# Optimization experiments

Measured on AMD Instinct MI355X. Metric: run time of the kernel, lower is better.

Reference implementation:

```python
import jax, jax.numpy as jnp
import numpy as np

B, T, H, OUT_LEN, D_IN, D_OUT = 512, 512, 256, 8, 64, 64

def _lstm_seq(x, Wih, Whh, bih, bhh):
    # batch_first LSTM, zero initial state; x: [B,T,D] -> [B,T,H]
    b = bih + bhh
    h0 = jnp.zeros((x.shape[0], Whh.shape[1]), x.dtype)
    def step(carry, xt):
        h, c = carry
        g = xt @ Wih.T + h @ Whh.T + b
        i, f, gg, o = jnp.split(g, 4, axis=-1)  # torch gate order i,f,g,o
        c = jax.nn.sigmoid(f) * c + jax.nn.sigmoid(i) * jnp.tanh(gg)
        h = jax.nn.sigmoid(o) * jnp.tanh(c)
        return (h, c), h
    _, hs = jax.lax.scan(step, (h0, h0), jnp.swapaxes(x, 0, 1))
    return jnp.swapaxes(hs, 0, 1)

def _lstm_cell0(xt, Wih, bih, bhh):
    # single decode step; original calls self.dec with fresh zero (h,c) each
    # step, so the recurrent matrix Whh never contributes.
    g = xt @ Wih.T + bih + bhh
    i, f, gg, o = jnp.split(g, 4, axis=-1)
    c = jax.nn.sigmoid(i) * jnp.tanh(gg)
    return jax.nn.sigmoid(o) * jnp.tanh(c)

def _mlp(x, Ws, bs, Wl, bl):
    # simple.mlp: hidden Linear+ReLU stack, linear output (dropout off)
    for k in range(Ws.shape[0]):
        x = jax.nn.relu(x @ Ws[k] + bs[k])
    return x @ Wl + bl

def setup_inputs():
    key = jax.random.key(0)
    ks = iter(jax.random.split(key, 32))
    def W(shape, fan):
        return jax.random.normal(next(ks), shape, jnp.float32) / np.float32(np.sqrt(fan))
    return {
        'x': jax.random.normal(next(ks), (B, T, D_IN), jnp.float32),
        'in_W': W((D_IN, H), D_IN), 'in_b': jnp.zeros((H,), jnp.float32),
        'enc_Wih': W((4*H, H), H), 'enc_Whh': W((4*H, H), H),
        'enc_bih': jnp.zeros((4*H,), jnp.float32), 'enc_bhh': jnp.zeros((4*H,), jnp.float32),
        'dec_Wih': W((4*H, 2*H), 2*H), 'dec_Whh': W((4*H, H), H),
        'dec_bih': jnp.zeros((4*H,), jnp.float32), 'dec_bhh': jnp.zeros((4*H,), jnp.float32),
        'w_Ws': W((3, H, H), H), 'w_bs': jnp.zeros((3, H), jnp.float32), 'w_Wl': W((H, H), H), 'w_bl': jnp.zeros((H,), jnp.float32),
        'u_Ws': W((3, H, H), H), 'u_bs': jnp.zeros((3, H), jnp.float32), 'u_Wl': W((H, H), H), 'u_bl': jnp.zeros((H,), jnp.float32),
        'v_Ws': W((7, H, H), H), 'v_bs': jnp.zeros((7, H), jnp.float32), 'v_Wl': W((H, 1), H), 'v_bl': jnp.zeros((1,), jnp.float32),
        'out_W': W((H, D_OUT), H), 'out_b': jnp.zeros((D_OUT,), jnp.float32),
    }

def reference(x, in_W, in_b, enc_Wih, enc_Whh, enc_bih, enc_bhh,
              dec_Wih, dec_Whh, dec_bih, dec_bhh,
              w_Ws, w_bs, w_Wl, w_bl, u_Ws, u_bs, u_Wl, u_bl,
              v_Ws, v_bs, v_Wl, v_bl, out_W, out_b):
    h = x @ in_W + in_b                                       # input projection [B,T,H]
    enc = _lstm_seq(h, enc_Wih, enc_Whh, enc_bih, enc_bhh)    # [B,T,H]
    whs = _mlp(enc, w_Ws, w_bs, w_Wl, w_bl)                   # w(hs), loop-invariant (hoisted)
    def dec_step(s, _):
        us = _mlp(s, u_Ws, u_bs, u_Wl, u_bl)                  # [B,H]
        e = _mlp(jnp.tanh(us[:, None, :] + whs), v_Ws, v_bs, v_Wl, v_bl)  # [B,T,1]
        a = jax.nn.softmax(e, axis=1)                         # softmax over time
        c_t = jnp.sum(a * enc, axis=1)                        # [B,H] weighted sum
        s_new = _lstm_cell0(jnp.concatenate([c_t, s], axis=-1), dec_Wih, dec_bih, dec_bhh)
        return s_new, s_new
    s0 = jnp.zeros((x.shape[0], H), x.dtype)
    _, ss = jax.lax.scan(dec_step, s0, None, length=OUT_LEN)  # [OUT_LEN,B,H]
    dec = jnp.swapaxes(ss, 0, 1)                              # [B,OUT_LEN,H]
    return dec @ out_W + out_b                                # output projection
```

## Files before the change

### kernel.cpp

```cpp
#include <hip/hip_runtime.h>
#include <math.h>

#define B_    512
#define T_    512
#define H_    256
#define DIN_  64
#define OL_   8
#define DOUT_ 64

#define CBv   128
#define HSTR  32768

typedef unsigned short u16;
typedef unsigned int u32;
typedef unsigned long long ull;
typedef __attribute__((ext_vector_type(8))) short short8;
typedef __attribute__((ext_vector_type(4))) float f32x4;

static __device__ __forceinline__ float sigm(float x){ return 1.0f/(1.0f + expf(-x)); }
static __device__ __forceinline__ float bf2f(u16 h){
  u32 u = ((u32)h) << 16; float f; __builtin_memcpy(&f, &u, 4); return f;
}
static __device__ __forceinline__ u16 f2bf(float f){
  u32 u; __builtin_memcpy(&u, &f, 4);
  u = (u + 0x7fffu + ((u >> 16) & 1u)) >> 16;
  return (u16)u;
}
static __device__ __forceinline__ u32 packhl(float f){
  u16 h = f2bf(f);
  u16 lo = f2bf(f - bf2f(h));
  return ((u32)h << 16) | (u32)lo;
}
static __device__ __forceinline__ float unpackhl(u32 w){
  return bf2f((u16)(w >> 16)) + bf2f((u16)(w & 0xffff));
}
static __device__ __forceinline__ u32 al(const u32* p){
  return __hip_atomic_load(p, __ATOMIC_RELAXED, __HIP_MEMORY_SCOPE_AGENT);
}
static __device__ __forceinline__ void as_(u32* p, u32 v){
  __hip_atomic_store(p, v, __ATOMIC_RELAXED, __HIP_MEMORY_SCOPE_AGENT);
}

__global__ void k_wpt(const float* __restrict__ inW, const float* __restrict__ Wih,
                      float* __restrict__ WpT)
{
  int gid = blockIdx.x * 256 + threadIdx.x;
  int c = gid >> 6, d = gid & 63;
  const float* wr = Wih + c * H_;
  const float* ir = inW + d * H_;
  float acc = 0.f;
  #pragma unroll 4
  for (int e = 0; e < H_; e += 4) {
    float4 av = *(const float4*)(ir + e);
    float4 bv = *(const float4*)(wr + e);
    acc += av.x*bv.x + av.y*bv.y + av.z*bv.z + av.w*bv.w;
  }
  WpT[c*64 + d] = acc;
}

__global__ void k_bp(const float* __restrict__ inb, const float* __restrict__ Wih,
                     const float* __restrict__ bih, const float* __restrict__ bhh,
                     float* __restrict__ bp)
{
  int c = blockIdx.x * 256 + threadIdx.x;
  const float* wr = Wih + c * H_;
  float acc = bih[c] + bhh[c];
  for (int e = 0; e < H_; ++e) acc += inb[e] * wr[e];
  bp[c] = acc;
}

__global__ void k_dwt(const float* __restrict__ dWih, float* __restrict__ dWt)
{
  int gid = blockIdx.x * 256 + threadIdx.x;
  int j = gid >> 9, k = gid & 511;
  int row = (j < 256) ? j : (j + 256);
  dWt[k*768 + j] = dWih[row*512 + k];
}

__global__ void k_wall(const float* __restrict__ wWs, const float* __restrict__ wWl,
                       const float* __restrict__ uWs, const float* __restrict__ uWl,
                       const float* __restrict__ vWs, u16* __restrict__ outb)
{
  int lyr = blockIdx.y;
  const float* W = (lyr < 3)  ? wWs + lyr*65536
                 : (lyr == 3) ? wWl
                 : (lyr < 7)  ? uWs + (lyr-4)*65536
                 : (lyr == 7) ? uWl
                 :              vWs + (lyr-8)*65536;
  u16* out = outb + (size_t)lyr*131072;
  int gid = blockIdx.x * 256 + threadIdx.x;
  int k = gid & 255, n = gid >> 8;
  float v = W[k*256 + n];
  int s = k >> 5, j = k & 7;
  int lane = (((k >> 3) & 3) << 4) | (n & 15);
  int fl = ((s*16) + (n >> 4))*512 + lane*8 + j;
  u16 h = f2bf(v);
  out[fl] = h;
  out[65536 + fl] = f2bf(v - bf2f(h));
}

__global__ void k_whhfl(const float* __restrict__ Whh, u16* __restrict__ out)
{
  int gid = blockIdx.x * 256 + threadIdx.x;
  int j = gid & 7, l = (gid >> 3) & 63, ctg = (gid >> 9) & 63, s = gid >> 15;
  int k = s*32 + (l >> 4)*8 + j;
  int wv = ctg >> 2, g = ctg & 3;
  int row = g*256 + wv*16 + (l & 15);
  float v = Whh[row*256 + k];
  int fl = (s*64 + ctg)*512 + l*8 + j;
  u16 h = f2bf(v);
  out[fl] = h;
  out[262144 + fl] = f2bf(v - bf2f(h));
}

__global__ void k_wpfl(const float* __restrict__ WpT, u16* __restrict__ out)
{
  int gid = blockIdx.x * 256 + threadIdx.x;
  int j = gid & 7, l = (gid >> 3) & 63, ctg = (gid >> 9) & 63, s = gid >> 15;
  int k = s*32 + (l >> 4)*8 + j;
  int wv = ctg >> 2, g = ctg & 3;
  int row = g*256 + wv*16 + (l & 15);
  float v = WpT[row*64 + k];
  int fl = (s*64 + ctg)*512 + l*8 + j;
  u16 h = f2bf(v);
  out[fl] = h;
  out[65536 + fl] = f2bf(v - bf2f(h));
}

__global__ __launch_bounds__(256,1) void k_enc(
    const float* __restrict__ x, const u16* __restrict__ whhFL,
    const u16* __restrict__ wpFL, const float* __restrict__ bp,
    u32* __restrict__ henc)
{
  __shared__ float G[2][16][32][4];
  const int tid = threadIdx.x, l = tid & 63, wv = tid >> 6;
  const int lr = l & 15, lk = l >> 4;
  const int rg = blockIdx.x, bg = blockIdx.y, z = blockIdx.z;
  const int ug2 = wv >> 1;
  const int g0 = (wv & 1) * 2;
  const int u16g = bg*2 + ug2;

  short8 whH[8][2], whL[8][2], wpH[2][2], wpL[2][2];
  #pragma unroll
  for (int s = 0; s < 8; ++s)
    #pragma unroll
    for (int c = 0; c < 2; ++c) {
      int ctg = u16g*4 + g0 + c;
      whH[s][c] = *(const short8*)(whhFL + ((size_t)(s*64 + ctg))*512 + l*8);
      whL[s][c] = *(const short8*)(whhFL + 262144 + ((size_t)(s*64 + ctg))*512 + l*8);
    }
  #pragma unroll
  for (int s = 0; s < 2; ++s)
    #pragma unroll
    for (int c = 0; c < 2; ++c) {
      int ctg = u16g*4 + g0 + c;
      wpH[s][c] = *(const short8*)(wpFL + ((size_t)(s*64 + ctg))*512 + l*8);
      wpL[s][c] = *(const short8*)(wpFL + 65536 + ((size_t)(s*64 + ctg))*512 + l*8);
    }
  const int ul = tid & 31, er0 = tid >> 5;
  float bb[4];
  #pragma unroll
  for (int g = 0; g < 4; ++g) bb[g] = bp[g*256 + bg*32 + ul];
  float cs[2] = {0.f, 0.f};

  u32* hz = henc + (size_t)z * (size_t)(T_+1) * HSTR;
  const float* xrow = x + ((size_t)(z*CBv + rg*16 + lr)*T_)*DIN_ + lk*8;

  for (int t = 0; t < T_; ++t) {
    float4 xv0 = *(const float4*)(xrow);
    float4 xv1 = *(const float4*)(xrow + 4);
    float4 xv2 = *(const float4*)(xrow + 32);
    float4 xv3 = *(const float4*)(xrow + 36);
    xrow += DIN_;

    const ull* hb = (const ull*)(hz + (size_t)t*HSTR + (size_t)(rg*16 + lr)*256);
    ull hq[8][4];
    #pragma unroll
    for (int s = 0; s < 8; ++s)
      #pragma unroll
      for (int q = 0; q < 4; ++q)
        hq[s][q] = __hip_atomic_load(hb + s*16 + lk*4 + q,
                                     __ATOMIC_RELAXED, __HIP_MEMORY_SCOPE_AGENT);
    if (t) {
      for (;;) {
        bool ok = true;
        #pragma unroll
        for (int s = 0; s < 8; ++s)
          #pragma unroll
          for (int q = 0; q < 4; ++q) {
            u32 a = (u32)hq[s][q], b = (u32)(hq[s][q] >> 32);
            ok = ok && (a != 0u) && (b != 0u);
          }
        if (__all(ok)) break;
        __builtin_amdgcn_s_sleep(1);
        #pragma unroll
        for (int s = 0; s < 8; ++s)
          #pragma unroll
          for (int q = 0; q < 4; ++q)
            hq[s][q] = __hip_atomic_load(hb + s*16 + lk*4 + q,
                                         __ATOMIC_RELAXED, __HIP_MEMORY_SCOPE_AGENT);
      }
    }

    f32x4 acc[2];
    acc[0] = (f32x4){0.f,0.f,0.f,0.f};
    acc[1] = (f32x4){0.f,0.f,0.f,0.f};

    #pragma unroll
    for (int s = 0; s < 2; ++s) {
      float vv[8];
      if (s == 0) { vv[0]=xv0.x;vv[1]=xv0.y;vv[2]=xv0.z;vv[3]=xv0.w;vv[4]=xv1.x;vv[5]=xv1.y;vv[6]=xv1.z;vv[7]=xv1.w; }
      else        { vv[0]=xv2.x;vv[1]=xv2.y;vv[2]=xv2.z;vv[3]=xv2.w;vv[4]=xv3.x;vv[5]=xv3.y;vv[6]=xv3.z;vv[7]=xv3.w; }
      short8 ah, al2;
      #pragma unroll
      for (int j = 0; j < 8; ++j) {
        u16 h = f2bf(vv[j]);
        ah[j] = (short)h;
        al2[j] = (short)f2bf(vv[j] - bf2f(h));
      }
      #pragma unroll
      for (int c = 0; c < 2; ++c) {
        acc[c] = __builtin_amdgcn_mfma_f32_16x16x32_bf16(ah,  wpH[s][c], acc[c], 0,0,0);
        acc[c] = __builtin_amdgcn_mfma_f32_16x16x32_bf16(al2, wpH[s][c], acc[c], 0,0,0);
        acc[c] = __builtin_amdgcn_mfma_f32_16x16x32_bf16(ah,  wpL[s][c], acc[c], 0,0,0);
      }
    }
    #pragma unroll
    for (int s = 0; s < 8; ++s) {
      short8 ah, al2;
      #pragma unroll
      for (int q = 0; q < 4; ++q) {
        u32 w0 = (u32)hq[s][q], w1 = (u32)(hq[s][q] >> 32);
        ah[q*2]   = (short)(w0 >> 16); al2[q*2]   = (short)(w0 & 0xffff);
        ah[q*2+1] = (short)(w1 >> 16); al2[q*2+1] = (short)(w1 & 0xffff);
      }
      #pragma unroll
      for (int c = 0; c < 2; ++c) {
        acc[c] = __builtin_amdgcn_mfma_f32_16x16x32_bf16(ah,  whH[s][c], acc[c], 0,0,0);
        acc[c] = __builtin_amdgcn_mfma_f32_16x16x32_bf16(al2, whH[s][c], acc[c], 0,0,0);
        acc[c] = __builtin_amdgcn_mfma_f32_16x16x32_bf16(ah,  whL[s][c], acc[c], 0,0,0);
      }
    }

    const int p = t & 1;
    #pragma unroll
    for (int c = 0; c < 2; ++c)
      #pragma unroll
      for (int j = 0; j < 4; ++j)
        G[p][lk*4 + j][ug2*16 + lr][g0 + c] = acc[c][j];
    __syncthreads();

    #pragma unroll
    for (int pp = 0; pp < 2; ++pp) {
      int row = er0 + pp*8;
      float4 gq = *(const float4*)&G[p][row][ul][0];
      float gi = gq.x + bb[0], gf = gq.y + bb[1];
      float gg = gq.z + bb[2], go = gq.w + bb[3];
      float cn = sigm(gf)*cs[pp] + sigm(gi)*tanhf(gg);
      float hn = sigm(go)*tanhf(cn);
      cs[pp] = cn;
      as_(hz + (size_t)(t+1)*HSTR + (size_t)(rg*16 + row)*256 + bg*32 + ul,
          packhl(hn) | 1u);
    }
  }
}

static __device__ __forceinline__ void mlp_core(
    u32* act, const u16* wFL, const float* bs, const float* bl,
    int L, int nbs, bool lastRelu, int tid)
{
  const int l = tid & 63, cg = tid >> 6;
  const int lr = l & 15, lk = l >> 4;
  f32x4 acc[4][2];
  for (int lyr = 0; lyr < L; ++lyr) {
    __syncthreads();
    const u16* wb = wFL + (size_t)lyr*131072;
    #pragma unroll
    for (int rt = 0; rt < 4; ++rt)
      #pragma unroll
      for (int ct = 0; ct < 2; ++ct) acc[rt][ct] = (f32x4){0.f,0.f,0.f,0.f};

    short8 bh[3][2], blo[3][2];
    #pragma unroll
    for (int pre = 0; pre < 2; ++pre)
      #pragma unroll
      for (int ct = 0; ct < 2; ++ct) {
        const u16* bfp = wb + ((size_t)(pre*16 + cg*2 + ct))*512 + l*8;
        bh[pre][ct]  = *(const short8*)bfp;
        blo[pre][ct] = *(const short8*)(bfp + 65536);
      }
    #pragma unroll
    for (int s = 0; s < 8; ++s) {
      const int cur = s % 3, nxt = (s + 2) % 3;
      if (s < 6) {
        #pragma unroll
        for (int ct = 0; ct < 2; ++ct) {
          const u16* bfp = wb + ((size_t)((s+2)*16 + cg*2 + ct))*512 + l*8;
          bh[nxt][ct]  = *(const short8*)bfp;
          blo[nxt][ct] = *(const short8*)(bfp + 65536);
        }
      }
      short8 ah[4], al2[4];
      #pragma unroll
      for (int rt = 0; rt < 4; ++rt) {
        int row = rt*16 + lr;
        int cc = s*8 + lk*2;
        const u32* base = act + row*256;
        uint4 d0 = *(const uint4*)(base + (((cc    ) ^ (row & 7)) << 2));
        uint4 d1 = *(const uint4*)(base + (((cc + 1) ^ (row & 7)) << 2));
        u32 q[8] = {d0.x,d0.y,d0.z,d0.w,d1.x,d1.y,d1.z,d1.w};
        #pragma unroll
        for (int j = 0; j < 8; ++j) {
          ah[rt][j]  = (short)(q[j] >> 16);
          al2[rt][j] = (short)(q[j] & 0xffff);
        }
      }
      #pragma unroll
      for (int ct = 0; ct < 2; ++ct)
        #pragma unroll
        for (int rt = 0; rt < 4; ++rt) {
          acc[rt][ct] = __builtin_amdgcn_mfma_f32_16x16x32_bf16(ah[rt],  bh[cur][ct],  acc[rt][ct], 0,0,0);
          acc[rt][ct] = __builtin_amdgcn_mfma_f32_16x16x32_bf16(al2[rt], bh[cur][ct],  acc[rt][ct], 0,0,0);
          acc[rt][ct] = __builtin_amdgcn_mfma_f32_16x16x32_bf16(ah[rt],  blo[cur][ct], acc[rt][ct], 0,0,0);
        }
    }
    const float* bptr = (lyr < nbs) ? (bs + lyr*256) : bl;
    const bool dorelu = (lyr < L-1) || lastRelu;
    #pragma unroll
    for (int ct = 0; ct < 2; ++ct) {
      float bv = bptr[cg*32 + ct*16 + lr];
      #pragma unroll
      for (int rt = 0; rt < 4; ++rt)
        #pragma unroll
        for (int g = 0; g < 4; ++g) {
          float xv = acc[rt][ct][g] + bv;
          acc[rt][ct][g] = dorelu ? fmaxf(xv, 0.f) : xv;
        }
    }
    __syncthreads();
    #pragma unroll
    for (int ct = 0; ct < 2; ++ct) {
      int n = cg*32 + ct*16 + lr;
      #pragma unroll
      for (int rt = 0; rt < 4; ++rt)
        #pragma unroll
        for (int g = 0; g < 4; ++g) {
          int row = rt*16 + lk*4 + g;
          act[row*256 + (((n >> 2) ^ (row & 7)) << 2) + (n & 3)] = packhl(acc[rt][ct][g]);
        }
    }
  }
  __syncthreads();
}

__global__ __launch_bounds__(512,1) void k_dec_all(
    const u32* __restrict__ henc, const u16* __restrict__ mlpFL,
    const float* __restrict__ wbs, const float* __restrict__ wbl,
    const float* __restrict__ ubs, const float* __restrict__ ubl,
    const float* __restrict__ vbs, const float* __restrict__ vWl,
    const float* __restrict__ vbl,
    const float* __restrict__ dWt, const float* __restrict__ dbih,
    const float* __restrict__ dbhh,
    const float* __restrict__ oW, const float* __restrict__ ob,
    u32* __restrict__ whsP,
    u32* __restrict__ eS, u32* __restrict__ ctxS, u32* __restrict__ sS,
    float* __restrict__ outc)
{
  extern __shared__ u32 act[];
  __shared__ float red[8], red2[8];
  const int bid = blockIdx.x, tid = threadIdx.x;
  u32* usL = act + 16384;
  const u16* wFLw = mlpFL;
  const u16* wFLu = mlpFL + 4*131072;
  const u16* wFLv = mlpFL + 8*131072;
  const int half = bid & 1;
  const bool useW = (whsP != nullptr);
  float sprev[4] = {0.f, 0.f, 0.f, 0.f};

  if (useW) {
    for (int k = 0; k < 4; ++k) {
      long m0t = (long)(bid + 256*k) * 64;
      __syncthreads();
      for (int i = tid; i < 4096; i += 512) {
        int row = i >> 6, c16 = i & 63;
        uint4 pk = *(const uint4*)(henc + HSTR + (m0t + row)*256 + c16*4);
        *((uint4*)(act + row*256 + ((c16 ^ (row & 7)) << 2))) = pk;
      }
      mlp_core(act, wFLw, wbs, wbl, 4, 3, false, tid);
      for (int i = tid; i < 4096; i += 512) {
        int row = i >> 6, c16 = i & 63;
        uint4 pk = *((const uint4*)(act + row*256 + ((c16 ^ (row & 7)) << 2)));
        *(uint4*)(whsP + (m0t + row)*256 + c16*4) = pk;
      }
    }
  }

  for (int s = 0; s < OL_; ++s) {
    __syncthreads();
    for (int i = tid; i < 4096; i += 512) {
      int row = i >> 6, c16 = i & 63;
      uint4 pk;
      if (s) {
        const u32* sp = sS + (size_t)s*32768 + (size_t)(half*64 + row)*256 + c16*4;
        u32 w0 = al(sp), w1 = al(sp+1), w2 = al(sp+2), w3 = al(sp+3);
        while (!(w0 && w1 && w2 && w3)) {
          __builtin_amdgcn_s_sleep(1);
          w0 = al(sp); w1 = al(sp+1); w2 = al(sp+2); w3 = al(sp+3);
        }
        pk = (uint4){ packhl(__uint_as_float(w0)), packhl(__uint_as_float(w1)),
                      packhl(__uint_as_float(w2)), packhl(__uint_as_float(w3)) };
      } else {
        pk = (uint4){0u, 0u, 0u, 0u};
      }
      *((uint4*)(act + row*256 + ((c16 ^ (row & 7)) << 2))) = pk;
    }
    mlp_core(act, wFLu, ubs, ubl, 4, 3, false, tid);
    for (int i = tid; i < 16384; i += 512) usL[i] = act[i];

    for (int k = 0; k < 4; ++k) {
      long m0t = (long)(bid + 256*k) * 64;
      __syncthreads();
      if (useW) {
        for (int i = tid; i < 4096; i += 512) {
          int row = i >> 6, c16 = i & 63;
          uint4 pw = *(const uint4*)(whsP + (m0t + row)*256 + c16*4);
          u32* dst = act + row*256 + ((c16 ^ (row & 7)) << 2);
          const u32* uw = usL + row*256 + ((c16 ^ (row & 7)) << 2);
          dst[0] = packhl(tanhf(unpackhl(pw.x) + unpackhl(uw[0])));
          dst[1] = packhl(tanhf(unpackhl(pw.y) + unpackhl(uw[1])));
          dst[2] = packhl(tanhf(unpackhl(pw.z) + unpackhl(uw[2])));
          dst[3] = packhl(tanhf(unpackhl(pw.w) + unpackhl(uw[3])));
        }
      } else {
        for (int i = tid; i < 4096; i += 512) {
          int row = i >> 6, c16 = i & 63;
          uint4 pk = *(const uint4*)(henc + HSTR + (m0t + row)*256 + c16*4);
          *((uint4*)(act + row*256 + ((c16 ^ (row & 7)) << 2))) = pk;
        }
        mlp_core(act, wFLw, wbs, wbl, 4, 3, false, tid);
        for (int i = tid; i < 16384; i += 512) {
          u32 a = act[i], u = usL[i];
          act[i] = packhl(tanhf(unpackhl(a) + unpackhl(u)));
        }
      }
      mlp_core(act, wFLv, vbs, vbs, 7, 7, true, tid);
      {
        int r2 = tid >> 3, q = tid & 7;
        float p = 0.f;
        #pragma unroll 8
        for (int j = 0; j < 32; ++j) {
          int n = q*32 + j;
          u32 w = act[r2*256 + (((n >> 2) ^ (r2 & 7)) << 2) + (n & 3)];
          p += unpackhl(w) * vWl[n];
        }
        p += __shfl_xor(p, 1, 64);
        p += __shfl_xor(p, 2, 64);
        p += __shfl_xor(p, 4, 64);
        if (q == 0)
          as_(eS + (size_t)s*65536 + m0t + r2, __float_as_uint(p + vbl[0]) | 1u);
      }
    }

    if (bid >= 64 && bid < 192) {
      int b = bid - 64;
      __syncthreads();
      float* asx = (float*)act;
      const u32* ep0 = eS + (size_t)s*65536 + b;
      u32 w0;
      for (;;) {
        w0 = al(ep0 + (size_t)tid*128);
        if (w0) break;
        __builtin_amdgcn_s_sleep(1);
      }
      float v0 = __uint_as_float(w0);
      const int lane = tid & 63, wv = tid >> 6;
      float m = v0;
      #pragma unroll
      for (int o = 32; o; o >>= 1) m = fmaxf(m, __shfl_xor(m, o, 64));
      if (!lane) red[wv] = m;
      __syncthreads();
      m = fmaxf(fmaxf(fmaxf(red[0], red[1]), fmaxf(red[2], red[3])),
                fmaxf(fmaxf(red[4], red[5]), fmaxf(red[6], red[7])));
      float x0 = expf(v0 - m);
      float sm = x0;
      #pragma unroll
      for (int o = 32; o; o >>= 1) sm += __shfl_xor(sm, o, 64);
      if (!lane) red2[wv] = sm;
      __syncthreads();
      float inv = 1.f / (red2[0] + red2[1] + red2[2] + red2[3]
                       + red2[4] + red2[5] + red2[6] + red2[7]);
      asx[tid] = x0 * inv;
      __syncthreads();
      int unit = tid & 255, hf = tid >> 8;
      float accv = 0.f;
      const u32* hp = henc + HSTR + (size_t)b*256 + unit;
      #pragma unroll 8
      for (int t = hf*256; t < hf*256 + 256; ++t)
        accv += asx[t] * unpackhl(hp[(size_t)t*HSTR]);
      float* part = asx + 512;
      part[tid] = accv;
      __syncthreads();
      if (hf == 0)
        as_(ctxS + (size_t)s*32768 + b*256 + unit,
            __float_as_uint(accv + part[256 + unit]) | 1u);
    }

    if (bid >= 224) {
      int c = bid - 224, b0r = c*4;
      __syncthreads();
      float* xt = (float*)act;
      const int u = tid & 255, kh = tid >> 8;
      if (kh == 0) {
        const u32* cp = ctxS + (size_t)s*32768 + (size_t)b0r*256 + u;
        u32 w0, w1, w2, w3;
        for (;;) {
          w0 = al(cp); w1 = al(cp + 256); w2 = al(cp + 512); w3 = al(cp + 768);
          if (w0 && w1 && w2 && w3) break;
          __builtin_amdgcn_s_sleep(1);
        }
        xt[0*520 + u] = __uint_as_float(w0);
        xt[1*520 + u] = __uint_as_float(w1);
        xt[2*520 + u] = __uint_as_float(w2);
        xt[3*520 + u] = __uint_as_float(w3);
        #pragma unroll
        for (int bb = 0; bb < 4; ++bb) xt[bb*520 + 256 + u] = sprev[bb];
      }
      __syncthreads();
      float ai[4], ag[4], ao[4];
      #pragma unroll
      for (int bb = 0; bb < 4; ++bb) { ai[bb]=0.f; ag[bb]=0.f; ao[bb]=0.f; }
      #pragma unroll 4
      for (int k = kh*256; k < kh*256 + 256; ++k) {
        float wi = dWt[k*768 + u];
        float wg = dWt[k*768 + 256 + u];
        float wo = dWt[k*768 + 512 + u];
        #pragma unroll
        for (int bb = 0; bb < 4; ++bb) {
          float xv = xt[bb*520 + k];
          ai[bb] += xv*wi; ag[bb] += xv*wg; ao[bb] += xv*wo;
        }
      }
      float* pr = xt + 4*520;
      if (kh) {
        #pragma unroll
        for (int bb = 0; bb < 4; ++bb) {
          pr[(0*4 + bb)*256 + u] = ai[bb];
          pr[(1*4 + bb)*256 + u] = ag[bb];
          pr[(2*4 + bb)*256 + u] = ao[bb];
        }
      }
      __syncthreads();
      float* sn = pr + 3*4*256;
      if (!kh) {
        float bi = dbih[u]       + dbhh[u];
        float bg = dbih[512 + u] + dbhh[512 + u];
        float bo = dbih[768 + u] + dbhh[768 + u];
        #pragma unroll
        for (int bb = 0; bb < 4; ++bb) {
          float a1 = ai[bb] + pr[(0*4 + bb)*256 + u];
          float g1 = ag[bb] + pr[(1*4 + bb)*256 + u];
          float o1 = ao[bb] + pr[(2*4 + bb)*256 + u];
          float cn = sigm(a1 + bi) * tanhf(g1 + bg);
          float hn = sigm(o1 + bo) * tanhf(cn);
          as_(sS + (size_t)(s+1)*32768 + (size_t)(b0r + bb)*256 + u,
              __float_as_uint(hn) | 1u);
          sprev[bb] = hn;
          sn[bb*256 + u] = hn;
        }
      }
      __syncthreads();
      if (tid < 256) {
        int d = tid & 63, rr = tid >> 6;
        float a2 = ob[d];
        #pragma unroll 4
        for (int k = 0; k < 256; ++k) a2 += sn[rr*256 + k] * oW[k*64 + d];
        outc[((size_t)(b0r + rr)*OL_ + s)*64 + d] = a2;
      }
    }
  }
}

extern "C" void kernel_launch(void* const* d_in, const int* in_sizes, int n_in,
                              void* d_out, int out_size, void* d_ws, size_t ws_size,
                              hipStream_t stream)
{
  (void)in_sizes; (void)n_in;
  const float* x    = (const float*)d_in[0];
  const float* inW  = (const float*)d_in[1];
  const float* inb  = (const float*)d_in[2];
  const float* eWih = (const float*)d_in[3];
  const float* eWhh = (const float*)d_in[4];
  const float* ebih = (const float*)d_in[5];
  const float* ebhh = (const float*)d_in[6];
  const float* dWih = (const float*)d_in[7];
  const float* dbih = (const float*)d_in[9];
  const float* dbhh = (const float*)d_in[10];
  const float* wWs  = (const float*)d_in[11];
  const float* wbs  = (const float*)d_in[12];
  const float* wWl  = (const float*)d_in[13];
  const float* wbl  = (const float*)d_in[14];
  const float* uWs  = (const float*)d_in[15];
  const float* ubs  = (const float*)d_in[16];
  const float* uWl  = (const float*)d_in[17];
  const float* ubl  = (const float*)d_in[18];
  const float* vWs  = (const float*)d_in[19];
  const float* vbs  = (const float*)d_in[20];
  const float* vWl  = (const float*)d_in[21];
  const float* vbl  = (const float*)d_in[22];
  const float* oW   = (const float*)d_in[23];
  const float* ob   = (const float*)d_in[24];
  float* out = (float*)d_out;

  hipFuncSetAttribute((const void*)k_dec_all, hipFuncAttributeMaxDynamicSharedMemorySize, 131072);

  const size_t hsz = (size_t)(T_+1) * HSTR;
  const size_t avail = ws_size / 4;
  const size_t scratchU = 524288ull + 262144 + 294912;
  const size_t prepsU = 1770496ull;
  auto needf = [&](int nc, int usewhs) -> size_t {
    return (size_t)nc*hsz + (usewhs ? 16777216ull : 0ull) + scratchU + prepsU + 4096;
  };
  int NC = 1, USEW = 0;
  if      (needf(4,1) <= avail) { NC = 4; USEW = 1; }
  else if (needf(4,0) <= avail) { NC = 4; USEW = 0; }
  else if (needf(2,1) <= avail) { NC = 2; USEW = 1; }
  else if (needf(1,1) <= avail) { NC = 1; USEW = 1; }
  else if (needf(1,0) <= avail) { NC = 1; USEW = 0; }
  else { hipMemsetAsync(d_out, 0, (size_t)out_size*4, stream); return; }

  float* wsf = (float*)d_ws;
  size_t o = 0;
  u32* henc = (u32*)(wsf + o);  o += (size_t)NC*hsz;
  u32* whsP = nullptr;
  if (USEW) { whsP = (u32*)(wsf + o);  o += 16777216; }
  u32* eS   = (u32*)(wsf + o);  o += 524288;
  u32* ctxS = (u32*)(wsf + o);  o += 262144;
  u32* sS   = (u32*)(wsf + o);  o += 294912;
  float* WpT = wsf + o;  o += 65536;
  float* bp  = wsf + o;  o += 1024;
  float* dWt = wsf + o;  o += 393216;
  u16* whhFL = (u16*)(wsf + o);  o += 262144;
  u16* wpFL  = (u16*)(wsf + o);  o += 65536;
  u16* mlpFL = (u16*)(wsf + o);

  const size_t scratchBytes = scratchU * 4;

  k_wpt<<<256, 256, 0, stream>>>(inW, eWih, WpT);
  k_bp <<<4,   256, 0, stream>>>(inb, eWih, ebih, ebhh, bp);
  k_dwt<<<1536,256, 0, stream>>>(dWih, dWt);
  k_whhfl<<<1024,256,0,stream>>>(eWhh, whhFL);
  k_wpfl <<<256, 256,0,stream>>>(WpT, wpFL);
  k_wall <<<dim3(256,15), 256, 0, stream>>>(wWs, wWl, uWs, uWl, vWs, mlpFL);

  for (int c0 = 0; c0 < B_; c0 += CBv*NC) {
    hipMemsetAsync(henc, 0, (size_t)NC*hsz*4, stream);

    k_enc<<<dim3(CBv/16, 8, NC), 256, 0, stream>>>(
        x + (size_t)c0*T_*DIN_, whhFL, wpFL, bp, henc);

    for (int z = 0; z < NC; ++z) {
      hipMemsetAsync(eS, 0, scratchBytes, stream);
      k_dec_all<<<256, 512, 131072, stream>>>(
          henc + (size_t)z*hsz, mlpFL,
          wbs, wbl, ubs, ubl, vbs, vWl, vbl,
          dWt, dbih, dbhh, oW, ob,
          whsP, eS, ctxS, sS,
          out + (size_t)(c0 + z*CBv)*OL_*DOUT_);
    }
  }
}
```

Measured before the change: 16.64 ms.

## Store MLP activations as split hi/lo bf16 planes in shared memory

Replaces the packed hi|lo u32 activation layout in LDS with two separate bf16 planes, swizzled in 8-element groups. MFMA A operands can then be loaded directly as short8 vectors instead of being unpacked from u32 words on every k-step. All producers and consumers (loads, tanh combine, u-state copy, final dot) are adapted to the new layout. It also stops selecting the 4-chunk encoder configuration and falls back to at most 2 chunks, which may reduce encoder parallelism.

```diff
diff --git a/kernel.cpp b/kernel.cpp
--- a/kernel.cpp
+++ b/kernel.cpp
@@ -266,7 +266,7 @@
 }
 
 static __device__ __forceinline__ void mlp_core(
-    u32* act, const u16* wFL, const float* bs, const float* bl,
+    u16* hi, u16* lo, const u16* wFL, const float* bs, const float* bl,
     int L, int nbs, bool lastRelu, int tid)
 {
   const int l = tid & 63, cg = tid >> 6;
@@ -304,16 +304,9 @@
       #pragma unroll
       for (int rt = 0; rt < 4; ++rt) {
         int row = rt*16 + lr;
-        int cc = s*8 + lk*2;
-        const u32* base = act + row*256;
-        uint4 d0 = *(const uint4*)(base + (((cc    ) ^ (row & 7)) << 2));
-        uint4 d1 = *(const uint4*)(base + (((cc + 1) ^ (row & 7)) << 2));
-        u32 q[8] = {d0.x,d0.y,d0.z,d0.w,d1.x,d1.y,d1.z,d1.w};
-        #pragma unroll
-        for (int j = 0; j < 8; ++j) {
-          ah[rt][j]  = (short)(q[j] >> 16);
-          al2[rt][j] = (short)(q[j] & 0xffff);
-        }
+        int gs = (s*4 + lk) ^ ((row & 7) << 2);
+        ah[rt]  = *(const short8*)(hi + row*256 + gs*8);
+        al2[rt] = *(const short8*)(lo + row*256 + gs*8);
       }
       #pragma unroll
       for (int ct = 0; ct < 2; ++ct)
@@ -346,7 +339,11 @@
         #pragma unroll
         for (int g = 0; g < 4; ++g) {
           int row = rt*16 + lk*4 + g;
-          act[row*256 + (((n >> 2) ^ (row & 7)) << 2) + (n & 3)] = packhl(acc[rt][ct][g]);
+          int a = row*256 + (((n >> 3) ^ ((row & 7) << 2)) << 3) + (n & 7);
+          float xv = acc[rt][ct][g];
+          u16 h = f2bf(xv);
+          hi[a] = h;
+          lo[a] = f2bf(xv - bf2f(h));
         }
     }
   }
@@ -369,7 +366,10 @@
   extern __shared__ u32 act[];
   __shared__ float red[8], red2[8];
   const int bid = blockIdx.x, tid = threadIdx.x;
-  u32* usL = act + 16384;
+  u16* hiA = (u16*)act;
+  u16* loA = hiA + 16384;
+  u16* hiU = hiA + 32768;
+  u16* loU = hiA + 49152;
   const u16* wFLw = mlpFL;
   const u16* wFLu = mlpFL + 4*131072;
   const u16* wFLv = mlpFL + 8*131072;
@@ -381,77 +381,135 @@
     for (int k = 0; k < 4; ++k) {
       long m0t = (long)(bid + 256*k) * 64;
       __syncthreads();
-      for (int i = tid; i < 4096; i += 512) {
-        int row = i >> 6, c16 = i & 63;
-        uint4 pk = *(const uint4*)(henc + HSTR + (m0t + row)*256 + c16*4);
-        *((uint4*)(act + row*256 + ((c16 ^ (row & 7)) << 2))) = pk;
-      }
-      mlp_core(act, wFLw, wbs, wbl, 4, 3, false, tid);
-      for (int i = tid; i < 4096; i += 512) {
-        int row = i >> 6, c16 = i & 63;
-        uint4 pk = *((const uint4*)(act + row*256 + ((c16 ^ (row & 7)) << 2)));
-        *(uint4*)(whsP + (m0t + row)*256 + c16*4) = pk;
+      for (int i = tid; i < 2048; i += 512) {
+        int row = i >> 5, g8 = i & 31;
+        const u32* src = henc + HSTR + (m0t + row)*256 + g8*8;
+        uint4 a0 = *(const uint4*)src, a1 = *(const uint4*)(src + 4);
+        u32 w[8] = {a0.x,a0.y,a0.z,a0.w,a1.x,a1.y,a1.z,a1.w};
+        short8 hv, lv;
+        #pragma unroll
+        for (int j = 0; j < 8; ++j) { hv[j] = (short)(w[j] >> 16); lv[j] = (short)(w[j] & 0xffff); }
+        int gs = g8 ^ ((row & 7) << 2);
+        *(short8*)(hiA + row*256 + gs*8) = hv;
+        *(short8*)(loA + row*256 + gs*8) = lv;
+      }
+      mlp_core(hiA, loA, wFLw, wbs, wbl, 4, 3, false, tid);
+      for (int i = tid; i < 2048; i += 512) {
+        int row = i >> 5, g8 = i & 31;
+        int gs = g8 ^ ((row & 7) << 2);
+        short8 hv = *(const short8*)(hiA + row*256 + gs*8);
+        short8 lv = *(const short8*)(loA + row*256 + gs*8);
+        u32 w[8];
+        #pragma unroll
+        for (int j = 0; j < 8; ++j) w[j] = ((u32)(u16)hv[j] << 16) | (u32)(u16)lv[j];
+        u32* dst = whsP + (m0t + row)*256 + g8*8;
+        *(uint4*)dst       = (uint4){w[0],w[1],w[2],w[3]};
+        *(uint4*)(dst + 4) = (uint4){w[4],w[5],w[6],w[7]};
       }
     }
   }
 
   for (int s = 0; s < OL_; ++s) {
     __syncthreads();
-    for (int i = tid; i < 4096; i += 512) {
-      int row = i >> 6, c16 = i & 63;
-      uint4 pk;
+    for (int i = tid; i < 2048; i += 512) {
+      int row = i >> 5, g8 = i & 31;
+      short8 hv, lv;
       if (s) {
-        const u32* sp = sS + (size_t)s*32768 + (size_t)(half*64 + row)*256 + c16*4;
-        u32 w0 = al(sp), w1 = al(sp+1), w2 = al(sp+2), w3 = al(sp+3);
-        while (!(w0 && w1 && w2 && w3)) {
+        const u32* sp = sS + (size_t)s*32768 + (size_t)(half*64 + row)*256 + g8*8;
+        u32 w[8];
+        for (;;) {
+          bool ok = true;
+          #pragma unroll
+          for (int j = 0; j < 8; ++j) { w[j] = al(sp + j); ok = ok && (w[j] != 0u); }
+          if (ok) break;
           __builtin_amdgcn_s_sleep(1);
-          w0 = al(sp); w1 = al(sp+1); w2 = al(sp+2); w3 = al(sp+3);
-        }
-        pk = (uint4){ packhl(__uint_as_float(w0)), packhl(__uint_as_float(w1)),
-                      packhl(__uint_as_float(w2)), packhl(__uint_as_float(w3)) };
+        }
+        #pragma unroll
+        for (int j = 0; j < 8; ++j) {
+          float v = __uint_as_float(w[j]);
+          u16 h = f2bf(v);
+          hv[j] = (short)h;
+          lv[j] = (short)f2bf(v - bf2f(h));
+        }
       } else {
-        pk = (uint4){0u, 0u, 0u, 0u};
-      }
-      *((uint4*)(act + row*256 + ((c16 ^ (row & 7)) << 2))) = pk;
-    }
-    mlp_core(act, wFLu, ubs, ubl, 4, 3, false, tid);
-    for (int i = tid; i < 16384; i += 512) usL[i] = act[i];
+        #pragma unroll
+        for (int j = 0; j < 8; ++j) { hv[j] = 0; lv[j] = 0; }
+      }
+      int gs = g8 ^ ((row & 7) << 2);
+      *(short8*)(hiA + row*256 + gs*8) = hv;
+      *(short8*)(loA + row*256 + gs*8) = lv;
+    }
+    mlp_core(hiA, loA, wFLu, ubs, ubl, 4, 3, false, tid);
+    for (int i = tid; i < 16384; i += 512) act[16384 + i] = act[i];
+    __syncthreads();
 
     for (int k = 0; k < 4; ++k) {
       long m0t = (long)(bid + 256*k) * 64;
       __syncthreads();
       if (useW) {
-        for (int i = tid; i < 4096; i += 512) {
-          int row = i >> 6, c16 = i & 63;
-          uint4 pw = *(const uint4*)(whsP + (m0t + row)*256 + c16*4);
-          u32* dst = act + row*256 + ((c16 ^ (row & 7)) << 2);
-          const u32* uw = usL + row*256 + ((c16 ^ (row & 7)) << 2);
-          dst[0] = packhl(tanhf(unpackhl(pw.x) + unpackhl(uw[0])));
-          dst[1] = packhl(tanhf(unpackhl(pw.y) + unpackhl(uw[1])));
-          dst[2] = packhl(tanhf(unpackhl(pw.z) + unpackhl(uw[2])));
-          dst[3] = packhl(tanhf(unpackhl(pw.w) + unpackhl(uw[3])));
+        for (int i = tid; i < 2048; i += 512) {
+          int row = i >> 5, g8 = i & 31;
+          int gs = g8 ^ ((row & 7) << 2);
+          const u32* src = whsP + (m0t + row)*256 + g8*8;
+          uint4 a0 = *(const uint4*)src, a1 = *(const uint4*)(src + 4);
+          u32 w[8] = {a0.x,a0.y,a0.z,a0.w,a1.x,a1.y,a1.z,a1.w};
+          short8 uh = *(const short8*)(hiU + row*256 + gs*8);
+          short8 ul = *(const short8*)(loU + row*256 + gs*8);
+          short8 hv, lv;
+          #pragma unroll
+          for (int j = 0; j < 8; ++j) {
+            float v = tanhf(unpackhl(w[j]) + bf2f((u16)uh[j]) + bf2f((u16)ul[j]));
+            u16 h = f2bf(v);
+            hv[j] = (short)h;
+            lv[j] = (short)f2bf(v - bf2f(h));
+          }
+          *(short8*)(hiA + row*256 + gs*8) = hv;
+          *(short8*)(loA + row*256 + gs*8) = lv;
         }
       } else {
-        for (int i = tid; i < 4096; i += 512) {
-          int row = i >> 6, c16 = i & 63;
-          uint4 pk = *(const uint4*)(henc + HSTR + (m0t + row)*256 + c16*4);
-          *((uint4*)(act + row*256 + ((c16 ^ (row & 7)) << 2))) = pk;
-        }
-        mlp_core(act, wFLw, wbs, wbl, 4, 3, false, tid);
-        for (int i = tid; i < 16384; i += 512) {
-          u32 a = act[i], u = usL[i];
-          act[i] = packhl(tanhf(unpackhl(a) + unpackhl(u)));
-        }
-      }
-      mlp_core(act, wFLv, vbs, vbs, 7, 7, true, tid);
+        for (int i = tid; i < 2048; i += 512) {
+          int row = i >> 5, g8 = i & 31;
+          const u32* src = henc + HSTR + (m0t + row)*256 + g8*8;
+          uint4 a0 = *(const uint4*)src, a1 = *(const uint4*)(src + 4);
+          u32 w[8] = {a0.x,a0.y,a0.z,a0.w,a1.x,a1.y,a1.z,a1.w};
+          short8 hv, lv;
+          #pragma unroll
+          for (int j = 0; j < 8; ++j) { hv[j] = (short)(w[j] >> 16); lv[j] = (short)(w[j] & 0xffff); }
+          int gs = g8 ^ ((row & 7) << 2);
+          *(short8*)(hiA + row*256 + gs*8) = hv;
+          *(short8*)(loA + row*256 + gs*8) = lv;
+        }
+        mlp_core(hiA, loA, wFLw, wbs, wbl, 4, 3, false, tid);
+        for (int i = tid; i < 2048; i += 512) {
+          int row = i >> 5, g8 = i & 31;
+          int gs = g8 ^ ((row & 7) << 2);
+          short8 av = *(const short8*)(hiA + row*256 + gs*8);
+          short8 bv = *(const short8*)(loA + row*256 + gs*8);
+          short8 uh = *(const short8*)(hiU + row*256 + gs*8);
+          short8 ul = *(const short8*)(loU + row*256 + gs*8);
+          short8 hv, lv;
+          #pragma unroll
+          for (int j = 0; j < 8; ++j) {
+            float v = tanhf(bf2f((u16)av[j]) + bf2f((u16)bv[j])
+                          + bf2f((u16)uh[j]) + bf2f((u16)ul[j]));
+            u16 h = f2bf(v);
+            hv[j] = (short)h;
+            lv[j] = (short)f2bf(v - bf2f(h));
+          }
+          *(short8*)(hiA + row*256 + gs*8) = hv;
+          *(short8*)(loA + row*256 + gs*8) = lv;
+        }
+        __syncthreads();
+      }
+      mlp_core(hiA, loA, wFLv, vbs, vbs, 7, 7, true, tid);
       {
         int r2 = tid >> 3, q = tid & 7;
         float p = 0.f;
         #pragma unroll 8
         for (int j = 0; j < 32; ++j) {
           int n = q*32 + j;
-          u32 w = act[r2*256 + (((n >> 2) ^ (r2 & 7)) << 2) + (n & 3)];
-          p += unpackhl(w) * vWl[n];
+          int a = r2*256 + (((n >> 3) ^ ((r2 & 7) << 2)) << 3) + (n & 7);
+          p += (bf2f(hiA[a]) + bf2f(loA[a])) * vWl[n];
         }
         p += __shfl_xor(p, 1, 64);
         p += __shfl_xor(p, 2, 64);
@@ -621,9 +679,7 @@
     return (size_t)nc*hsz + (usewhs ? 16777216ull : 0ull) + scratchU + prepsU + 4096;
   };
   int NC = 1, USEW = 0;
-  if      (needf(4,1) <= avail) { NC = 4; USEW = 1; }
-  else if (needf(4,0) <= avail) { NC = 4; USEW = 0; }
-  else if (needf(2,1) <= avail) { NC = 2; USEW = 1; }
+  if      (needf(2,1) <= avail) { NC = 2; USEW = 1; }
   else if (needf(1,1) <= avail) { NC = 1; USEW = 1; }
   else if (needf(1,0) <= avail) { NC = 1; USEW = 0; }
   else { hipMemsetAsync(d_out, 0, (size_t)out_size*4, stream); return; }
```

Result: slower. 17.00 ms (+2.2%).
